# Kernel optimization log

Hardware: AMD Instinct MI355X
Metric: run time of the kernel (lower is better)

The kernel has to match this reference:

```python
import jax, jax.numpy as jnp
import numpy as np

D_MODEL = 768
N_HEADS = 12
D_K = D_MODEL // N_HEADS
BATCH = 1
SEQ = 4096


def setup_inputs() -> dict:
    key = jax.random.key(0)
    kx, kq, kk, kv, ko = jax.random.split(key, 5)
    s = 1.0 / np.sqrt(D_MODEL)
    return {
        "x": jax.random.normal(kx, (BATCH, SEQ, D_MODEL), dtype=jnp.float32),
        "wq": jax.random.normal(kq, (D_MODEL, D_MODEL), dtype=jnp.float32) * s,
        "wk": jax.random.normal(kk, (D_MODEL, D_MODEL), dtype=jnp.float32) * s,
        "wv": jax.random.normal(kv, (D_MODEL, D_MODEL), dtype=jnp.float32) * s,
        "wo": jax.random.normal(ko, (D_MODEL, D_MODEL), dtype=jnp.float32) * s,
    }


def reference(x, wq, wk, wv, wo):
    B, S, D = x.shape
    H, dk = N_HEADS, D_K
    # nn.Linear(x) = x @ W.T ; reshape to [B,H,S,dk]
    def proj(w):
        return (x @ w.T).reshape(B, S, H, dk).transpose(0, 2, 1, 3)
    q, k, v = proj(wq), proj(wk), proj(wv)
    scores = jnp.einsum('bhqd,bhkd->bhqk', q, k) / np.sqrt(dk).astype(np.float32)
    attn = jax.nn.softmax(scores, axis=-1)
    out = jnp.einsum('bhqk,bhkd->bhqd', attn, v)
    out = out.transpose(0, 2, 1, 3).reshape(B, S, D)
    return out @ wo.T
```

## Files before the change

### kernel.cpp

```cpp
#include <hip/hip_runtime.h>
#include <stdint.h>

#define SEQ 4096
#define DMODEL 768
#define NHEADS 12
#define DKH 64

typedef __attribute__((ext_vector_type(8))) short short8;
typedef __attribute__((ext_vector_type(4))) float floatx4;
typedef __attribute__((ext_vector_type(16))) float floatx16;

__device__ __forceinline__ unsigned short f2bf(float f) {
    unsigned int u = __float_as_uint(f);
    u += 0x7fffu + ((u >> 16) & 1u);
    return (unsigned short)(u >> 16);
}

__device__ __forceinline__ float exp2fast(float x) {
    return __builtin_amdgcn_exp2f(x);
}

__device__ __forceinline__ unsigned int cvt_pk_bf16(float lo, float hi) {
    unsigned int r;
    asm("v_cvt_pk_bf16_f32 %0, %1, %2" : "=v"(r) : "v"(lo), "v"(hi));
    return r;
}

__device__ __forceinline__ int swz(int row, int colb) {
    return colb ^ ((row & 7) << 4);
}

__device__ __forceinline__ void async_copy16(void* lds, const void* g) {
    __builtin_amdgcn_global_load_lds(
        (const __attribute__((address_space(1))) void*)g,
        (__attribute__((address_space(3))) void*)lds,
        16, 0, 0);
}

__global__ __launch_bounds__(256) void castk(const float* __restrict__ src,
                                             unsigned short* __restrict__ dst,
                                             int n4) {
    int i = blockIdx.x * 256 + threadIdx.x;
    if (i >= n4) return;
    float4 v = ((const float4*)src)[i];
    ushort4 o;
    o.x = f2bf(v.x); o.y = f2bf(v.y); o.z = f2bf(v.z); o.w = f2bf(v.w);
    ((ushort4*)dst)[i] = o;
}

__global__ __launch_bounds__(256) void castw(const float* __restrict__ w0,
                                             const float* __restrict__ w1,
                                             const float* __restrict__ w2,
                                             const float* __restrict__ w3,
                                             unsigned short* __restrict__ dst) {
    int b = blockIdx.x;
    int wsel = b / 576;
    int i = (b % 576) * 256 + threadIdx.x;
    const float* src = (wsel == 0) ? w0 : (wsel == 1) ? w1 : (wsel == 2) ? w2 : w3;
    float4 v = ((const float4*)src)[i];
    ushort4 o;
    o.x = f2bf(v.x); o.y = f2bf(v.y); o.z = f2bf(v.z); o.w = f2bf(v.w);
    ((ushort4*)(dst + (size_t)wsel * 589824))[i] = o;
}

#define STAGE_G(bsel, kb)                                                              \
    do {                                                                               \
        char* As_ = smem + (bsel) * 24576;                                             \
        _Pragma("unroll") for (int ii = 0; ii < 4; ii++) {                             \
            int o = ii * 4096 + t * 16;                                                \
            int row = o >> 7, colb = o & 127;                                          \
            async_copy16(As_ + ii * 4096 + wid * 1024,                                 \
                         (const char*)A + ((size_t)(rowBase + row) * DMODEL + (kb)) * 2 \
                             + swz(row, colb));                                        \
        }                                                                              \
        _Pragma("unroll") for (int ii = 0; ii < 2; ii++) {                             \
            int o = ii * 4096 + t * 16;                                                \
            int row = o >> 7, colb = o & 127;                                          \
            async_copy16(As_ + 16384 + ii * 4096 + wid * 1024,                         \
                         (const char*)B + ((size_t)(colBase + row) * DMODEL + (kb)) * 2 \
                             + swz(row, colb));                                        \
        }                                                                              \
    } while (0)

#define GEMM_COMPUTE(As, Bs)                                                           \
    do {                                                                               \
        short8 a_[4][2], b_[2][2];                                                     \
        _Pragma("unroll") for (int m = 0; m < 4; m++)                                  \
            _Pragma("unroll") for (int kk = 0; kk < 2; kk++) {                         \
                int row = wr * 64 + m * 16 + lr;                                       \
                int colb = kk * 64 + lg * 16;                                          \
                a_[m][kk] = *(const short8*)((As) + row * 128 + swz(row, colb));       \
            }                                                                          \
        _Pragma("unroll") for (int n = 0; n < 2; n++)                                  \
            _Pragma("unroll") for (int kk = 0; kk < 2; kk++) {                         \
                int row = wc * 32 + n * 16 + lr;                                       \
                int colb = kk * 64 + lg * 16;                                          \
                b_[n][kk] = *(const short8*)((Bs) + row * 128 + swz(row, colb));       \
            }                                                                          \
        _Pragma("unroll") for (int m = 0; m < 4; m++)                                  \
            _Pragma("unroll") for (int n = 0; n < 2; n++)                              \
                _Pragma("unroll") for (int kk = 0; kk < 2; kk++)                       \
                    acc[m][n] = __builtin_amdgcn_mfma_f32_16x16x32_bf16(               \
                        a_[m][kk], b_[n][kk], acc[m][n], 0, 0, 0);                     \
    } while (0)

__global__ __launch_bounds__(256, 2)
void gemm_qkv(const unsigned short* __restrict__ A,
              const unsigned short* __restrict__ W,
              unsigned short* __restrict__ OutBase, float qscale) {
    __shared__ __align__(128) char smem[49152];

    const int t = threadIdx.x;
    const int wid = t >> 6, lane = t & 63;
    const int lr = lane & 15, lg = lane >> 4;
    const int wr = wid >> 1, wc = wid & 1;
    const int rowBase = blockIdx.x * 128;
    const int proj = blockIdx.y / 12;
    const int colBase = (blockIdx.y % 12) * 64;
    const unsigned short* B = W + (size_t)proj * 589824;

    const floatx4 zero4 = {0.f, 0.f, 0.f, 0.f};
    floatx4 acc[4][2];
#pragma unroll
    for (int m = 0; m < 4; m++)
#pragma unroll
        for (int n = 0; n < 2; n++) acc[m][n] = zero4;

    STAGE_G(0, 0);
    for (int i = 0; i < 12; ++i) {
        __builtin_amdgcn_s_barrier();
        __builtin_amdgcn_sched_barrier(0);
        if (i < 11) {
            STAGE_G((i + 1) & 1, (i + 1) * 64);
            asm volatile("s_waitcnt vmcnt(6)" ::: "memory");
        } else {
            asm volatile("s_waitcnt vmcnt(0)" ::: "memory");
        }
        __builtin_amdgcn_s_barrier();
        __builtin_amdgcn_sched_barrier(0);
        char* As = smem + (i & 1) * 24576;
        GEMM_COMPUTE(As, As + 16384);
    }

    if (proj < 2) {
        unsigned short* O = OutBase + (size_t)proj * 3145728;
        float scale = (proj == 0) ? qscale : 1.0f;
#pragma unroll
        for (int m = 0; m < 4; m++)
#pragma unroll
            for (int n = 0; n < 2; n++)
#pragma unroll
                for (int r = 0; r < 4; r++) {
                    int srow = rowBase + wr * 64 + m * 16 + lg * 4 + r;
                    int col = colBase + wc * 32 + n * 16 + lr;
                    int h = col >> 6, d = col & 63;
                    O[((size_t)h * SEQ + srow) * DKH + d] = f2bf(acc[m][n][r] * scale);
                }
    } else {
        unsigned short* O = OutBase + 6291456;
#pragma unroll
        for (int m = 0; m < 4; m++)
#pragma unroll
            for (int n = 0; n < 2; n++) {
                int srow0 = rowBase + wr * 64 + m * 16 + lg * 4;
                int pos0 = (srow0 & ~15) | ((srow0 & 4) << 1) | ((srow0 & 8) >> 1);
                int col = colBase + wc * 32 + n * 16 + lr;
                ushort4 o4;
                o4.x = f2bf(acc[m][n][0]);
                o4.y = f2bf(acc[m][n][1]);
                o4.z = f2bf(acc[m][n][2]);
                o4.w = f2bf(acc[m][n][3]);
                *(ushort4*)(O + (size_t)col * SEQ + pos0) = o4;
            }
    }
}

__global__ __launch_bounds__(256, 2)
void gemm_o(const unsigned short* __restrict__ A,
            const unsigned short* __restrict__ B,
            float* __restrict__ Out) {
    __shared__ __align__(128) char smem[49152];

    const int t = threadIdx.x;
    const int wid = t >> 6, lane = t & 63;
    const int lr = lane & 15, lg = lane >> 4;
    const int wr = wid >> 1, wc = wid & 1;
    const int rowBase = blockIdx.x * 128;
    const int colBase = blockIdx.y * 64;

    const floatx4 zero4 = {0.f, 0.f, 0.f, 0.f};
    floatx4 acc[4][2];
#pragma unroll
    for (int m = 0; m < 4; m++)
#pragma unroll
        for (int n = 0; n < 2; n++) acc[m][n] = zero4;

    STAGE_G(0, 0);
    for (int i = 0; i < 12; ++i) {
        __builtin_amdgcn_s_barrier();
        __builtin_amdgcn_sched_barrier(0);
        if (i < 11) {
            STAGE_G((i + 1) & 1, (i + 1) * 64);
            asm volatile("s_waitcnt vmcnt(6)" ::: "memory");
        } else {
            asm volatile("s_waitcnt vmcnt(0)" ::: "memory");
        }
        __builtin_amdgcn_s_barrier();
        __builtin_amdgcn_sched_barrier(0);
        char* As = smem + (i & 1) * 24576;
        GEMM_COMPUTE(As, As + 16384);
    }

#pragma unroll
    for (int m = 0; m < 4; m++)
#pragma unroll
        for (int n = 0; n < 2; n++)
#pragma unroll
            for (int r = 0; r < 4; r++) {
                int srow = rowBase + wr * 64 + m * 16 + lg * 4 + r;
                int col = colBase + wc * 32 + n * 16 + lr;
                Out[(size_t)srow * DMODEL + col] = acc[m][n][r];
            }
}

__global__ __launch_bounds__(256, 3)
void attn_k(const unsigned short* __restrict__ Q,
            const unsigned short* __restrict__ Kp,
            const unsigned short* __restrict__ Vt,
            unsigned short* __restrict__ AO) {
    __shared__ __align__(128) char smem[49152];

    const int t = threadIdx.x;
    const int wid = t >> 6, lane = t & 63;
    const int q31 = lane & 31, hi = lane >> 5;
    const int e = wid;
    const int slot16 = (q31 * 2 + hi) * 16;

    int nid = (blockIdx.x & 7) * 96 + (blockIdx.x >> 3);
    const int h = nid >> 6, qb = nid & 63;
    const size_t headOff = (size_t)h * SEQ * DKH;

    short8 qf0[4], qf1[4];
    {
        const unsigned short* qp0 =
            Q + headOff + (size_t)(qb * 64 + q31) * DKH + hi * 8;
        const unsigned short* qp1 = qp0 + 32 * DKH;
#pragma unroll
        for (int ks = 0; ks < 4; ks++) {
            qf0[ks] = *(const short8*)(qp0 + ks * 16);
            qf1[ks] = *(const short8*)(qp1 + ks * 16);
        }
    }

    const char* ksrc[4];
    const char* vsrc[4];
#pragma unroll
    for (int ii = 0; ii < 4; ii++) {
        int cc = ii * 256 + wid * 64 + lane;
        int gk = cc >> 6, qd = (cc >> 1) & 31, hh = cc & 1;
        int kb2 = gk >> 2, ks2 = gk & 3;
        ksrc[ii] = (const char*)(Kp + headOff) + (size_t)(kb2 * 32 + qd) * 128
                   + (ks2 * 2 + hh) * 16;
        int fbv = gk & 1, cv = (gk >> 1) & 3, ev = gk >> 3;
        vsrc[ii] = (const char*)Vt
                   + ((size_t)(h * DKH + fbv * 32 + qd) * SEQ
                      + ev * 64 + cv * 16 + hh * 8) * 2;
    }

    const floatx16 z16 = {0.f, 0.f, 0.f, 0.f, 0.f, 0.f, 0.f, 0.f,
                          0.f, 0.f, 0.f, 0.f, 0.f, 0.f, 0.f, 0.f};
    float mrun[2] = {-3.0e38f, -3.0e38f}, lrun[2] = {0.f, 0.f};
    floatx16 accO[2][2] = {{z16, z16}, {z16, z16}};

#pragma unroll
    for (int ii = 0; ii < 4; ii++) {
        async_copy16(smem + (ii * 256 + wid * 64) * 16, ksrc[ii]);
        ksrc[ii] += 16384;
    }

    for (int tt = 0; tt < 32; ++tt) {
        asm volatile("s_waitcnt vmcnt(0)" ::: "memory");
        __builtin_amdgcn_s_barrier();
        __builtin_amdgcn_sched_barrier(0);
        {
            char* Vd = smem + 32768;
#pragma unroll
            for (int ii = 0; ii < 4; ii++) {
                async_copy16(Vd + (ii * 256 + wid * 64) * 16, vsrc[ii]);
                vsrc[ii] += 256;
            }
        }
        if (tt < 31) {
            char* Kd = smem + ((tt + 1) & 1) * 16384;
#pragma unroll
            for (int ii = 0; ii < 4; ii++) {
                async_copy16(Kd + (ii * 256 + wid * 64) * 16, ksrc[ii]);
                ksrc[ii] += 16384;
            }
        }
        __builtin_amdgcn_sched_barrier(0);

        const char* Ks = smem + (tt & 1) * 16384;
        const char* Vs = smem + 32768;

        floatx16 s0 = z16, s1 = z16;
        __builtin_amdgcn_s_setprio(1);
#pragma unroll
        for (int ks = 0; ks < 4; ks++) {
            short8 kf = *(const short8*)(Ks + (e * 4 + ks) * 1024 + slot16);
            s0 = __builtin_amdgcn_mfma_f32_32x32x16_bf16(kf, qf0[ks], s0, 0, 0, 0);
            s1 = __builtin_amdgcn_mfma_f32_32x32x16_bf16(kf, qf1[ks], s1, 0, 0, 0);
        }
        __builtin_amdgcn_s_setprio(0);

#pragma unroll
        for (int u = 0; u < 2; u++) {
            floatx16& s = (u == 0) ? s0 : s1;
            float a = fmaxf(fmaxf(s[0], s[1]), fmaxf(s[2], s[3]));
            float b = fmaxf(fmaxf(s[4], s[5]), fmaxf(s[6], s[7]));
            float c = fmaxf(fmaxf(s[8], s[9]), fmaxf(s[10], s[11]));
            float d = fmaxf(fmaxf(s[12], s[13]), fmaxf(s[14], s[15]));
            float mt = fmaxf(fmaxf(a, b), fmaxf(c, d));
            mt = fmaxf(mt, __shfl_xor(mt, 32));
            if (!__all(mt <= mrun[u] + 8.0f)) {
                float mnew = fmaxf(mrun[u], mt);
                float al = exp2fast(mrun[u] - mnew);
#pragma unroll
                for (int fb = 0; fb < 2; fb++)
#pragma unroll
                    for (int j = 0; j < 16; j++) accO[u][fb][j] *= al;
                lrun[u] *= al;
                mrun[u] = mnew;
            }
#pragma unroll
            for (int j = 0; j < 16; j++) s[j] = exp2fast(s[j] - mrun[u]);
            float sa = (s[0] + s[1]) + (s[2] + s[3]);
            float sb = (s[4] + s[5]) + (s[6] + s[7]);
            float sc = (s[8] + s[9]) + (s[10] + s[11]);
            float sd = (s[12] + s[13]) + (s[14] + s[15]);
            float sum = (sa + sb) + (sc + sd);
            sum += __shfl_xor(sum, 32);
            lrun[u] += sum;
        }

        if (tt < 31) asm volatile("s_waitcnt vmcnt(4)" ::: "memory");
        else         asm volatile("s_waitcnt vmcnt(0)" ::: "memory");
        __builtin_amdgcn_s_barrier();
        __builtin_amdgcn_sched_barrier(0);

        __builtin_amdgcn_s_setprio(1);
#pragma unroll
        for (int cp = 0; cp < 2; cp++) {
            const int r0 = cp * 8;
            uint4 pw0, pw1;
            pw0.x = cvt_pk_bf16(s0[r0 + 0], s0[r0 + 1]);
            pw0.y = cvt_pk_bf16(s0[r0 + 2], s0[r0 + 3]);
            pw0.z = cvt_pk_bf16(s0[r0 + 4], s0[r0 + 5]);
            pw0.w = cvt_pk_bf16(s0[r0 + 6], s0[r0 + 7]);
            pw1.x = cvt_pk_bf16(s1[r0 + 0], s1[r0 + 1]);
            pw1.y = cvt_pk_bf16(s1[r0 + 2], s1[r0 + 3]);
            pw1.z = cvt_pk_bf16(s1[r0 + 4], s1[r0 + 5]);
            pw1.w = cvt_pk_bf16(s1[r0 + 6], s1[r0 + 7]);
            short8 pf0 = *(const short8*)&pw0;
            short8 pf1 = *(const short8*)&pw1;
#pragma unroll
            for (int fb = 0; fb < 2; fb++) {
                int chunk = ((e >> 1) * 4 + (e & 1) * 2 + cp) * 2 + fb;
                short8 vf = *(const short8*)(Vs + chunk * 1024 + slot16);
                accO[0][fb] = __builtin_amdgcn_mfma_f32_32x32x16_bf16(vf, pf0, accO[0][fb], 0, 0, 0);
                accO[1][fb] = __builtin_amdgcn_mfma_f32_32x32x16_bf16(vf, pf1, accO[1][fb], 0, 0, 0);
            }
        }
        __builtin_amdgcn_s_setprio(0);
    }

    __builtin_amdgcn_s_barrier();
#define MSLOT(w, u) (smem + (((w) * 2 + (u)) * 64 + lane) * 160)
    if (e & 1) {
#pragma unroll
        for (int u = 0; u < 2; u++) {
            char* R = MSLOT(e >> 1, u);
#pragma unroll
            for (int fb = 0; fb < 2; fb++)
#pragma unroll
                for (int j4 = 0; j4 < 4; j4++) {
                    floatx4 v4 = {accO[u][fb][j4 * 4 + 0], accO[u][fb][j4 * 4 + 1],
                                  accO[u][fb][j4 * 4 + 2], accO[u][fb][j4 * 4 + 3]};
                    *(floatx4*)(R + fb * 64 + j4 * 16) = v4;
                }
            *(float*)(R + 128) = mrun[u];
            *(float*)(R + 132) = lrun[u];
        }
        asm volatile("s_waitcnt lgkmcnt(0)" ::: "memory");
    }
    __builtin_amdgcn_s_barrier();
    if (!(e & 1)) {
#pragma unroll
        for (int u = 0; u < 2; u++) {
            const char* R = MSLOT(e >> 1, u);
            float m1 = *(const float*)(R + 128);
            float l1 = *(const float*)(R + 132);
            float m = fmaxf(mrun[u], m1);
            float a0 = exp2fast(mrun[u] - m), a1 = exp2fast(m1 - m);
#pragma unroll
            for (int fb = 0; fb < 2; fb++)
#pragma unroll
                for (int j4 = 0; j4 < 4; j4++) {
                    floatx4 p4 = *(const floatx4*)(R + fb * 64 + j4 * 16);
#pragma unroll
                    for (int j = 0; j < 4; j++)
                        accO[u][fb][j4 * 4 + j] = accO[u][fb][j4 * 4 + j] * a0 + p4[j] * a1;
                }
            lrun[u] = lrun[u] * a0 + l1 * a1;
            mrun[u] = m;
        }
    }
    asm volatile("s_waitcnt lgkmcnt(0)" ::: "memory");
    __builtin_amdgcn_s_barrier();
    if (e == 2) {
#pragma unroll
        for (int u = 0; u < 2; u++) {
            char* R = MSLOT(0, u);
#pragma unroll
            for (int fb = 0; fb < 2; fb++)
#pragma unroll
                for (int j4 = 0; j4 < 4; j4++) {
                    floatx4 v4 = {accO[u][fb][j4 * 4 + 0], accO[u][fb][j4 * 4 + 1],
                                  accO[u][fb][j4 * 4 + 2], accO[u][fb][j4 * 4 + 3]};
                    *(floatx4*)(R + fb * 64 + j4 * 16) = v4;
                }
            *(float*)(R + 128) = mrun[u];
            *(float*)(R + 132) = lrun[u];
        }
        asm volatile("s_waitcnt lgkmcnt(0)" ::: "memory");
    }
    __builtin_amdgcn_s_barrier();
    if (e == 0) {
#pragma unroll
        for (int u = 0; u < 2; u++) {
            const char* R = MSLOT(0, u);
            float m1 = *(const float*)(R + 128);
            float l1 = *(const float*)(R + 132);
            float m = fmaxf(mrun[u], m1);
            float a0 = exp2fast(mrun[u] - m), a1 = exp2fast(m1 - m);
            float inv = 1.0f / (lrun[u] * a0 + l1 * a1);
            int srow = qb * 64 + u * 32 + q31;
#pragma unroll
            for (int fb = 0; fb < 2; fb++)
#pragma unroll
                for (int rq = 0; rq < 4; rq++) {
                    floatx4 p4 = *(const floatx4*)(R + fb * 64 + rq * 16);
                    ushort4 o4;
                    o4.x = f2bf((accO[u][fb][4 * rq + 0] * a0 + p4[0] * a1) * inv);
                    o4.y = f2bf((accO[u][fb][4 * rq + 1] * a0 + p4[1] * a1) * inv);
                    o4.z = f2bf((accO[u][fb][4 * rq + 2] * a0 + p4[2] * a1) * inv);
                    o4.w = f2bf((accO[u][fb][4 * rq + 3] * a0 + p4[3] * a1) * inv);
                    int col = h * DKH + fb * 32 + rq * 8 + hi * 4;
                    *(ushort4*)(AO + (size_t)srow * DMODEL + col) = o4;
                }
        }
    }
#undef MSLOT
}

extern "C" void kernel_launch(void* const* d_in, const int* in_sizes, int n_in,
                              void* d_out, int out_size, void* d_ws, size_t ws_size,
                              hipStream_t stream) {
    const float* x  = (const float*)d_in[0];
    const float* wq = (const float*)d_in[1];
    const float* wk = (const float*)d_in[2];
    const float* wv = (const float*)d_in[3];
    const float* wo = (const float*)d_in[4];

    char* ws = (char*)d_ws;
    unsigned short* xb  = (unsigned short*)(ws + 0);
    unsigned short* wqb = (unsigned short*)(ws + 6291456);
    unsigned short* wob = (unsigned short*)(ws + 9830400);
    unsigned short* Qb  = (unsigned short*)(ws + 11010048);
    unsigned short* Kb  = (unsigned short*)(ws + 17301504);
    unsigned short* VTb = (unsigned short*)(ws + 23592960);
    unsigned short* AOb = (unsigned short*)(ws + 29884416);

    castk<<<3072, 256, 0, stream>>>(x, xb, 786432);
    castw<<<2304, 256, 0, stream>>>(wq, wk, wv, wo, wqb);

    gemm_qkv<<<dim3(32, 36), 256, 0, stream>>>(xb, wqb, Qb, 0.18033688f);

    attn_k<<<dim3(768), 256, 0, stream>>>(Qb, Kb, VTb, AOb);

    gemm_o<<<dim3(32, 12), 256, 0, stream>>>(AOb, wob, (float*)d_out);
}
```

Baseline: 121.9 us.

## Load V fragments directly from global into registers, drop V LDS staging and barrier

V tiles were staged in LDS through async copies and read back after a second mid-iteration barrier. Each wave now loads its V^T fragments straight from global memory into registers at the start of the iteration, removing the V LDS buffer and the second s_waitcnt/barrier pair. K addressing is also simplified to a single base plus offset. Shared memory shrinks to 40 KB. The trade-off is that V global-load latency is now exposed within the iteration and register pressure rises.

```diff
diff --git a/kernel.cpp b/kernel.cpp
--- a/kernel.cpp
+++ b/kernel.cpp
@@ -228,7 +228,7 @@
             const unsigned short* __restrict__ Kp,
             const unsigned short* __restrict__ Vt,
             unsigned short* __restrict__ AO) {
-    __shared__ __align__(128) char smem[49152];
+    __shared__ __align__(128) char smem[40960];
 
     const int t = threadIdx.x;
     const int wid = t >> 6, lane = t & 63;
@@ -252,20 +252,12 @@
         }
     }
 
-    const char* ksrc[4];
-    const char* vsrc[4];
-#pragma unroll
-    for (int ii = 0; ii < 4; ii++) {
-        int cc = ii * 256 + wid * 64 + lane;
-        int gk = cc >> 6, qd = (cc >> 1) & 31, hh = cc & 1;
-        int kb2 = gk >> 2, ks2 = gk & 3;
-        ksrc[ii] = (const char*)(Kp + headOff) + (size_t)(kb2 * 32 + qd) * 128
-                   + (ks2 * 2 + hh) * 16;
-        int fbv = gk & 1, cv = (gk >> 1) & 3, ev = gk >> 3;
-        vsrc[ii] = (const char*)Vt
-                   + ((size_t)(h * DKH + fbv * 32 + qd) * SEQ
-                      + ev * 64 + cv * 16 + hh * 8) * 2;
-    }
+    const char* kbase = (const char*)(Kp + headOff);
+    int koff = (lane >> 1) * 128 + (wid * 2 + (lane & 1)) * 16;
+
+    const char* vbase = (const char*)Vt + (size_t)h * DKH * SEQ * 2;
+    int voff0 = (q31 * SEQ + (e >> 1) * 64 + (e & 1) * 32 + hi * 8) * 2;
+    int voff1 = voff0 + 32 * SEQ * 2;
 
     const floatx16 z16 = {0.f, 0.f, 0.f, 0.f, 0.f, 0.f, 0.f, 0.f,
                           0.f, 0.f, 0.f, 0.f, 0.f, 0.f, 0.f, 0.f};
@@ -273,35 +265,32 @@
     floatx16 accO[2][2] = {{z16, z16}, {z16, z16}};
 
 #pragma unroll
-    for (int ii = 0; ii < 4; ii++) {
-        async_copy16(smem + (ii * 256 + wid * 64) * 16, ksrc[ii]);
-        ksrc[ii] += 16384;
-    }
+    for (int ii = 0; ii < 4; ii++)
+        async_copy16(smem + ii * 4096 + wid * 1024, kbase + (koff + ii * 4096));
+    koff += 16384;
 
     for (int tt = 0; tt < 32; ++tt) {
         asm volatile("s_waitcnt vmcnt(0)" ::: "memory");
         __builtin_amdgcn_s_barrier();
         __builtin_amdgcn_sched_barrier(0);
-        {
-            char* Vd = smem + 32768;
-#pragma unroll
-            for (int ii = 0; ii < 4; ii++) {
-                async_copy16(Vd + (ii * 256 + wid * 64) * 16, vsrc[ii]);
-                vsrc[ii] += 256;
-            }
-        }
+
+        short8 vfa0 = *(const short8*)(vbase + voff0);
+        short8 vfa1 = *(const short8*)(vbase + voff0 + 32);
+        short8 vfb0 = *(const short8*)(vbase + voff1);
+        short8 vfb1 = *(const short8*)(vbase + voff1 + 32);
+        voff0 += 256; voff1 += 256;
+        __builtin_amdgcn_sched_barrier(0);
+
         if (tt < 31) {
             char* Kd = smem + ((tt + 1) & 1) * 16384;
 #pragma unroll
-            for (int ii = 0; ii < 4; ii++) {
-                async_copy16(Kd + (ii * 256 + wid * 64) * 16, ksrc[ii]);
-                ksrc[ii] += 16384;
-            }
+            for (int ii = 0; ii < 4; ii++)
+                async_copy16(Kd + ii * 4096 + wid * 1024, kbase + (koff + ii * 4096));
+            koff += 16384;
         }
         __builtin_amdgcn_sched_barrier(0);
 
         const char* Ks = smem + (tt & 1) * 16384;
-        const char* Vs = smem + 32768;
 
         floatx16 s0 = z16, s1 = z16;
         __builtin_amdgcn_s_setprio(1);
@@ -343,33 +332,40 @@
             lrun[u] += sum;
         }
 
-        if (tt < 31) asm volatile("s_waitcnt vmcnt(4)" ::: "memory");
-        else         asm volatile("s_waitcnt vmcnt(0)" ::: "memory");
-        __builtin_amdgcn_s_barrier();
-        __builtin_amdgcn_sched_barrier(0);
-
         __builtin_amdgcn_s_setprio(1);
-#pragma unroll
-        for (int cp = 0; cp < 2; cp++) {
-            const int r0 = cp * 8;
+        {
             uint4 pw0, pw1;
-            pw0.x = cvt_pk_bf16(s0[r0 + 0], s0[r0 + 1]);
-            pw0.y = cvt_pk_bf16(s0[r0 + 2], s0[r0 + 3]);
-            pw0.z = cvt_pk_bf16(s0[r0 + 4], s0[r0 + 5]);
-            pw0.w = cvt_pk_bf16(s0[r0 + 6], s0[r0 + 7]);
-            pw1.x = cvt_pk_bf16(s1[r0 + 0], s1[r0 + 1]);
-            pw1.y = cvt_pk_bf16(s1[r0 + 2], s1[r0 + 3]);
-            pw1.z = cvt_pk_bf16(s1[r0 + 4], s1[r0 + 5]);
-            pw1.w = cvt_pk_bf16(s1[r0 + 6], s1[r0 + 7]);
+            pw0.x = cvt_pk_bf16(s0[0], s0[1]);
+            pw0.y = cvt_pk_bf16(s0[2], s0[3]);
+            pw0.z = cvt_pk_bf16(s0[4], s0[5]);
+            pw0.w = cvt_pk_bf16(s0[6], s0[7]);
+            pw1.x = cvt_pk_bf16(s1[0], s1[1]);
+            pw1.y = cvt_pk_bf16(s1[2], s1[3]);
+            pw1.z = cvt_pk_bf16(s1[4], s1[5]);
+            pw1.w = cvt_pk_bf16(s1[6], s1[7]);
             short8 pf0 = *(const short8*)&pw0;
             short8 pf1 = *(const short8*)&pw1;
-#pragma unroll
-            for (int fb = 0; fb < 2; fb++) {
-                int chunk = ((e >> 1) * 4 + (e & 1) * 2 + cp) * 2 + fb;
-                short8 vf = *(const short8*)(Vs + chunk * 1024 + slot16);
-                accO[0][fb] = __builtin_amdgcn_mfma_f32_32x32x16_bf16(vf, pf0, accO[0][fb], 0, 0, 0);
-                accO[1][fb] = __builtin_amdgcn_mfma_f32_32x32x16_bf16(vf, pf1, accO[1][fb], 0, 0, 0);
-            }
+            accO[0][0] = __builtin_amdgcn_mfma_f32_32x32x16_bf16(vfa0, pf0, accO[0][0], 0, 0, 0);
+            accO[0][1] = __builtin_amdgcn_mfma_f32_32x32x16_bf16(vfb0, pf0, accO[0][1], 0, 0, 0);
+            accO[1][0] = __builtin_amdgcn_mfma_f32_32x32x16_bf16(vfa0, pf1, accO[1][0], 0, 0, 0);
+            accO[1][1] = __builtin_amdgcn_mfma_f32_32x32x16_bf16(vfb0, pf1, accO[1][1], 0, 0, 0);
+        }
+        {
+            uint4 pw0, pw1;
+            pw0.x = cvt_pk_bf16(s0[8], s0[9]);
+            pw0.y = cvt_pk_bf16(s0[10], s0[11]);
+            pw0.z = cvt_pk_bf16(s0[12], s0[13]);
+            pw0.w = cvt_pk_bf16(s0[14], s0[15]);
+            pw1.x = cvt_pk_bf16(s1[8], s1[9]);
+            pw1.y = cvt_pk_bf16(s1[10], s1[11]);
+            pw1.z = cvt_pk_bf16(s1[12], s1[13]);
+            pw1.w = cvt_pk_bf16(s1[14], s1[15]);
+            short8 pf0 = *(const short8*)&pw0;
+            short8 pf1 = *(const short8*)&pw1;
+            accO[0][0] = __builtin_amdgcn_mfma_f32_32x32x16_bf16(vfa1, pf0, accO[0][0], 0, 0, 0);
+            accO[0][1] = __builtin_amdgcn_mfma_f32_32x32x16_bf16(vfb1, pf0, accO[0][1], 0, 0, 0);
+            accO[1][0] = __builtin_amdgcn_mfma_f32_32x32x16_bf16(vfa1, pf1, accO[1][0], 0, 0, 0);
+            accO[1][1] = __builtin_amdgcn_mfma_f32_32x32x16_bf16(vfb1, pf1, accO[1][1], 0, 0, 0);
         }
         __builtin_amdgcn_s_setprio(0);
     }
```

Result: slower. 141.2 us (+15.8%).
